# Optimization experiments

Hardware: AMD Instinct MI355X
Metric: run time of the kernel (lower is better)

The kernel has to match this reference:

```python
import jax, jax.numpy as jnp
import numpy as np

B, N, D = 4, 2048, 512
H = 8
DH = D // H
FF = 2 * D


def setup_inputs() -> dict:
    key = jax.random.key(0)
    ks = jax.random.split(key, 16)
    s = lambda fan_in: 1.0 / np.sqrt(fan_in)
    inp = {
        "x0": jax.random.normal(ks[0], (B, N, D), jnp.float32),
        "x1": jax.random.normal(ks[1], (B, N, D), jnp.float32),
        # projections (torch Linear: weight [out, in])
        "Wqk": jax.random.uniform(ks[2], (D, D), jnp.float32, -s(D), s(D)),
        "bqk": jax.random.uniform(ks[3], (D,), jnp.float32, -s(D), s(D)),
        "Wv": jax.random.uniform(ks[4], (D, D), jnp.float32, -s(D), s(D)),
        "bv": jax.random.uniform(ks[5], (D,), jnp.float32, -s(D), s(D)),
        "Wo": jax.random.uniform(ks[6], (D, D), jnp.float32, -s(D), s(D)),
        "bo": jax.random.uniform(ks[7], (D,), jnp.float32, -s(D), s(D)),
        # FFN: Linear(2D,2D) -> LayerNorm(2D) -> GELU -> Linear(2D,D)
        "Wf1": jax.random.uniform(ks[8], (FF, FF), jnp.float32, -s(FF), s(FF)),
        "bf1": jax.random.uniform(ks[9], (FF,), jnp.float32, -s(FF), s(FF)),
        "ln_g": jnp.ones((FF,), jnp.float32),
        "ln_b": jnp.zeros((FF,), jnp.float32),
        "Wf2": jax.random.uniform(ks[10], (D, FF), jnp.float32, -s(FF), s(FF)),
        "bf2": jax.random.uniform(ks[11], (D,), jnp.float32, -s(FF), s(FF)),
    }
    return inp


def _split_heads(t):
    # [B,N,D] -> [B,H,N,DH]
    return t.reshape(B, N, H, DH).transpose(0, 2, 1, 3)


def _attn(q, k, v):
    # q,k,v: [B,H,N,DH]; scale by sqrt(d_k) as in the torch Attention module
    scores = jnp.einsum("bhnd,bhmd->bhnm", q, k) / jnp.sqrt(jnp.float32(DH))
    attn = jax.nn.softmax(scores, axis=-1)
    return jnp.einsum("bhnm,bhmd->bhnd", attn, v)


def _merge_heads(t):
    # [B,H,N,DH] -> [B,N,D]
    return t.transpose(0, 2, 1, 3).reshape(B, N, D)


def _ffn(x, Wf1, bf1, ln_g, ln_b, Wf2, bf2):
    h = x @ Wf1.T + bf1
    mu = jnp.mean(h, axis=-1, keepdims=True)
    var = jnp.mean(jnp.square(h - mu), axis=-1, keepdims=True)
    h = (h - mu) / jnp.sqrt(var + 1e-5) * ln_g + ln_b
    h = jax.nn.gelu(h, approximate=False)
    return h @ Wf2.T + bf2


def reference(x0, x1, Wqk, bqk, Wv, bv, Wo, bo, Wf1, bf1, ln_g, ln_b, Wf2, bf2):
    qk0 = _split_heads(x0 @ Wqk.T + bqk)
    qk1 = _split_heads(x1 @ Wqk.T + bqk)
    v0 = _split_heads(x0 @ Wv.T + bv)
    v1 = _split_heads(x1 @ Wv.T + bv)

    m0 = _merge_heads(_attn(qk0, qk1, v1)) @ Wo.T + bo
    m1 = _merge_heads(_attn(qk1, qk0, v0)) @ Wo.T + bo

    y0 = x0 + _ffn(jnp.concatenate([x0, m0], -1), Wf1, bf1, ln_g, ln_b, Wf2, bf2)
    y1 = x1 + _ffn(jnp.concatenate([x1, m1], -1), Wf1, bf1, ln_g, ln_b, Wf2, bf2)
    return (y0, y1)
```

## Files before the change

### kernel.cpp

```cpp
#include <hip/hip_runtime.h>
#include <hip/hip_bf16.h>
#include <math.h>

typedef __bf16 bf16;
typedef __bf16 bf16x8 __attribute__((ext_vector_type(8)));
typedef __bf16 bf16x4 __attribute__((ext_vector_type(4)));
typedef float  f32x4  __attribute__((ext_vector_type(4)));

#define DEVI __device__ __forceinline__

DEVI void async16(bf16* lds, const bf16* g) {
    __builtin_amdgcn_global_load_lds(
        (const __attribute__((address_space(1))) unsigned int*)g,
        (__attribute__((address_space(3))) unsigned int*)lds, 16, 0, 0);
}
DEVI f32x4 mfma16(bf16x8 a, bf16x8 b, f32x4 c) {
    return __builtin_amdgcn_mfma_f32_16x16x32_bf16(a, b, c, 0, 0, 0);
}

__global__ __launch_bounds__(256) void prep(
    const float* __restrict__ x0, const float* __restrict__ x1, bf16* __restrict__ Xbf,
    const float* __restrict__ Wqk, const float* __restrict__ Wv,
    const float* __restrict__ Wf1, const float* __restrict__ Wf2,
    bf16* __restrict__ Wqkv, bf16* __restrict__ Wbig, bf16* __restrict__ Wf1Rb,
    bf16* __restrict__ Wf2b,
    const float* __restrict__ Wo, bf16* __restrict__ WoT,
    const float* __restrict__ bo, const float* __restrict__ bf1,
    float* __restrict__ bf1p)
{
    __shared__ float Ls[64][65];
    const int bid = blockIdx.x, t = threadIdx.x;
    if (bid < 8192) {
        long i = (long)bid * 256 + t;
        long r = i >> 7, c = (i & 127) * 4;
        const float* src = (r < 8192) ? (x0 + r * 512 + c) : (x1 + (r - 8192) * 512 + c);
        float4 v = *(const float4*)src;
        bf16x4 o;
        o[0] = (bf16)v.x; o[1] = (bf16)v.y; o[2] = (bf16)v.z; o[3] = (bf16)v.w;
        *(bf16x4*)(Xbf + r * 1024 + c) = o;
    } else if (bid < 10240) {
        long i = (long)(bid - 8192) * 256 + t;
        const float* s; bf16* d;
        if (i < 131072) {
            s = (i < 65536) ? Wqk + i * 4 : Wv + (i - 65536) * 4;
            d = Wqkv + i * 4;
        } else if (i < 393216) {
            long e = (i - 131072) * 4, r = e >> 10, c = e & 1023;
            s = Wf1 + e;
            d = (c < 512) ? (Wbig + r * 1024 + c) : (Wf1Rb + r * 512 + (c - 512));
        } else {
            s = Wf2 + (i - 393216) * 4;
            d = Wf2b + (i - 393216) * 4;
        }
        float4 v = *(const float4*)s;
        bf16x4 o;
        o[0] = (bf16)v.x; o[1] = (bf16)v.y; o[2] = (bf16)v.z; o[3] = (bf16)v.w;
        *(bf16x4*)d = o;
    } else if (bid < 10304) {
        const int bb = bid - 10240;
        const int bi = bb & 7, bj = bb >> 3;
        const int i0 = bi * 64, j0 = bj * 64;
        const int r0 = t >> 4, c4 = (t & 15) * 4;
#pragma unroll
        for (int it = 0; it < 4; it++) {
            int row = r0 + 16 * it;
            float4 v = *(const float4*)(Wo + (long)(i0 + row) * 512 + j0 + c4);
            Ls[row][c4] = v.x; Ls[row][c4 + 1] = v.y;
            Ls[row][c4 + 2] = v.z; Ls[row][c4 + 3] = v.w;
        }
        __syncthreads();
#pragma unroll
        for (int it = 0; it < 4; it++) {
            int orow = r0 + 16 * it;
            bf16x4 o;
#pragma unroll
            for (int k = 0; k < 4; k++) o[k] = (bf16)Ls[c4 + k][orow];
            *(bf16x4*)(WoT + (long)(j0 + orow) * 512 + i0 + c4) = o;
        }
    } else {
        const int w = t >> 6, lane = t & 63;
        const int row = (bid - 10304) * 4 + w;
        const float* rp = Wf1 + (long)row * 1024 + 512 + lane * 8;
        float4 a = *(const float4*)rp;
        float4 b = *(const float4*)(rp + 4);
        const float* bp = bo + lane * 8;
        float4 c = *(const float4*)bp;
        float4 d = *(const float4*)(bp + 4);
        float s = a.x * c.x + a.y * c.y + a.z * c.z + a.w * c.w +
                  b.x * d.x + b.y * d.y + b.z * d.z + b.w * d.w;
#pragma unroll
        for (int k = 1; k < 64; k <<= 1) s += __shfl_xor(s, k);
        if (lane == 0) bf1p[row] = bf1[row] + s;
    }
}

template <int MODE>
__global__ __launch_bounds__(256) void gemm_bt(
    const bf16* __restrict__ A, long lda,
    const bf16* __restrict__ B, long ldb,
    const float* __restrict__ bias,
    void* __restrict__ Cout, long ldc,
    const float* __restrict__ res0, const float* __restrict__ res1,
    const float* __restrict__ bias2, void* __restrict__ Cout2,
    int M, int N, int K, float scale)
{
    __shared__ bf16 As[128 * 64];
    __shared__ bf16 Bs[128 * 64];
    const int t = threadIdx.x;
    const int w = t >> 6, lane = t & 63, quad = lane >> 4, m15 = lane & 15;
    const int wm = w >> 1, wn = w & 1;
    const int nbx = N >> 7;
    const int xcd = blockIdx.x & 7, local = blockIdx.x >> 3;
    const int mtiles_per_xcd = (int)(gridDim.x >> 3) / nbx;
    const int by = xcd * mtiles_per_xcd + local / nbx;
    const int bx = local % nbx;
    const long m0 = (long)by * 128, n0 = (long)bx * 128;

    f32x4 acc[4][4] = {};

    for (int k0 = 0; k0 < K; k0 += 64) {
#pragma unroll
        for (int i = 0; i < 4; i++) {
            int idx = i * 256 + t, row = idx >> 3, p = idx & 7;
            int gc = k0 + ((p ^ (row & 7)) * 8);
            async16(As + idx * 8, A + (m0 + row) * lda + gc);
            async16(Bs + idx * 8, B + (n0 + row) * ldb + gc);
        }
        __syncthreads();
#pragma unroll
        for (int kk = 0; kk < 2; kk++) {
            bf16x8 af[4], bfr[4];
#pragma unroll
            for (int mt = 0; mt < 4; mt++) {
                int row = wm * 64 + mt * 16 + m15;
                af[mt] = *(const bf16x8*)(As + row * 64 + (((kk * 4 + quad) ^ (row & 7)) * 8));
            }
#pragma unroll
            for (int nt = 0; nt < 4; nt++) {
                int row = wn * 64 + nt * 16 + m15;
                bfr[nt] = *(const bf16x8*)(Bs + row * 64 + (((kk * 4 + quad) ^ (row & 7)) * 8));
            }
#pragma unroll
            for (int mt = 0; mt < 4; mt++)
#pragma unroll
                for (int nt = 0; nt < 4; nt++)
                    acc[mt][nt] = mfma16(af[mt], bfr[nt], acc[mt][nt]);
        }
        __syncthreads();
    }

#pragma unroll
    for (int nt = 0; nt < 4; nt++) {
        long col = n0 + wn * 64 + nt * 16 + m15;
#pragma unroll
        for (int mt = 0; mt < 4; mt++) {
            long row = m0 + wm * 64 + mt * 16 + quad * 4;
            if (MODE == 0) {
                bf16* C = (bf16*)Cout;
                float bs = bias[col];
#pragma unroll
                for (int r = 0; r < 4; r++)
                    C[(row + r) * ldc + col] = (bf16)(acc[mt][nt][r] + bs);
            } else if (MODE == 4) {
                bf16* C = (bf16*)Cout;
#pragma unroll
                for (int r = 0; r < 4; r++)
                    C[(row + r) * ldc + col] = (bf16)acc[mt][nt][r];
            } else if (MODE == 5) {
                if (col < 512) {
                    bf16* C = (bf16*)Cout;
                    float bs = bias[col];
#pragma unroll
                    for (int r = 0; r < 4; r++)
                        C[(row + r) * ldc + col] = (bf16)((acc[mt][nt][r] + bs) * scale);
                } else {
                    bf16* V = (bf16*)Cout2;
                    long v = col - 512;
                    float bs = bias2[v];
                    bf16x4 pv;
#pragma unroll
                    for (int r = 0; r < 4; r++) pv[r] = (bf16)(acc[mt][nt][r] + bs);
                    *(bf16x4*)(V + v * 16384 + row) = pv;
                }
            } else {
                float* C = (float*)Cout;
                float bs = bias[col];
#pragma unroll
                for (int r = 0; r < 4; r++) {
                    long grow = row + r;
                    const float* rs = (grow < 8192) ? (res0 + grow * 512)
                                                    : (res1 + (grow - 8192) * 512);
                    C[grow * ldc + col] = acc[mt][nt][r] + bs + rs[col];
                }
            }
        }
    }
}

__global__ __launch_bounds__(256, 4) void flash_attn(const bf16* __restrict__ QK,
                                                     const bf16* __restrict__ VT,
                                                     bf16* __restrict__ o)
{
    __shared__ bf16 lds[20480];
    bf16* Ks = lds;
    bf16* Vs = lds + 8192;
    bf16* Ps = lds + 12288;

    const int t = threadIdx.x, w = t >> 6, lane = t & 63;
    const int quad = lane >> 4, m15 = lane & 15;
    const int bid = blockIdx.x;
    const int qt5 = bid & 15;
    const int h   = (bid >> 4) & 7;
    const int b   = (bid >> 7) & 3;
    const int dir = bid >> 9;
    const long qrow0  = (long)dir * 8192 + b * 2048 + qt5 * 128;
    const long kvrow0 = (long)(1 - dir) * 8192 + b * 2048;
    const int hc = h * 64;

#pragma unroll
    for (int i = 0; i < 4; i++) {
        int idx = i * 256 + t, row = idx >> 3, p = idx & 7;
        async16(lds + idx * 8, QK + (qrow0 + row) * 512 + hc + ((p ^ (row & 7)) * 8));
    }
    __syncthreads();
    bf16x8 qf[2][2];
#pragma unroll
    for (int qt = 0; qt < 2; qt++)
#pragma unroll
        for (int kh = 0; kh < 2; kh++) {
            int row = w * 32 + qt * 16 + m15;
            qf[qt][kh] = *(const bf16x8*)(lds + row * 64 + (((kh * 4 + quad) ^ (row & 7)) * 8));
        }
    __syncthreads();

#pragma unroll
    for (int i = 0; i < 2; i++) {
        int idx = i * 256 + t, row = idx >> 3, p = idx & 7;
        async16(Ks + idx * 8, QK + (kvrow0 + row) * 512 + hc + ((p ^ (row & 7)) * 8));
    }

    f32x4 oacc[4][2] = {};
    f32x4 racc[2] = {};
    bf16x8 ones;
#pragma unroll
    for (int j = 0; j < 8; j++) ones[j] = (bf16)1.0f;

    int cur = 0;
    for (int kb = 0; kb < 32; kb++) {
        const long key0  = kvrow0 + kb * 64;
        const long key0n = kvrow0 + ((kb + 1) & 31) * 64;
        bf16* Kc = Ks + cur * 4096;
        bf16* Kn = Ks + (cur ^ 1) * 4096;

        asm volatile("s_waitcnt vmcnt(0)" ::: "memory");
        __builtin_amdgcn_s_barrier();

#pragma unroll
        for (int i = 0; i < 2; i++) {
            int idx = i * 256 + t, row = idx >> 3, p = idx & 7;
            async16(Vs + idx * 8, VT + (long)(hc + row) * 16384 + key0 + ((p ^ (row & 7)) * 8));
        }
#pragma unroll
        for (int i = 0; i < 2; i++) {
            int idx = i * 256 + t, row = idx >> 3, p = idx & 7;
            async16(Kn + idx * 8, QK + (key0n + row) * 512 + hc + ((p ^ (row & 7)) * 8));
        }

        f32x4 s[4][2];
        __builtin_amdgcn_s_setprio(1);
#pragma unroll
        for (int mt = 0; mt < 4; mt++) {
            int row = mt * 16 + m15;
            bf16x8 kf0 = *(const bf16x8*)(Kc + row * 64 + ((quad ^ (row & 7)) * 8));
            bf16x8 kf1 = *(const bf16x8*)(Kc + row * 64 + (((4 + quad) ^ (row & 7)) * 8));
#pragma unroll
            for (int qt = 0; qt < 2; qt++) {
                f32x4 z = {0.f, 0.f, 0.f, 0.f};
                z = mfma16(kf0, qf[qt][0], z);
                s[mt][qt] = mfma16(kf1, qf[qt][1], z);
            }
        }
        __builtin_amdgcn_s_setprio(0);

#pragma unroll
        for (int qt = 0; qt < 2; qt++)
#pragma unroll
            for (int mt = 0; mt < 4; mt++)
#pragma unroll
                for (int r = 0; r < 4; r++)
                    s[mt][qt][r] = exp2f(s[mt][qt][r]);

        bf16* Pw = Ps + w * 2048;
#pragma unroll
        for (int qt = 0; qt < 2; qt++) {
            int ql = qt * 16 + m15;
#pragma unroll
            for (int mt = 0; mt < 4; mt++) {
                bf16x4 pv;
#pragma unroll
                for (int r = 0; r < 4; r++) pv[r] = (bf16)s[mt][qt][r];
                int u = (mt * 2 + (quad >> 1)) ^ (ql & 7);
                *(bf16x4*)(Pw + ql * 64 + u * 8 + (quad & 1) * 4) = pv;
            }
        }
        asm volatile("s_waitcnt vmcnt(2) lgkmcnt(0)" ::: "memory");
        __builtin_amdgcn_s_barrier();

        __builtin_amdgcn_s_setprio(1);
#pragma unroll
        for (int kc = 0; kc < 2; kc++) {
            bf16x8 pf[2];
#pragma unroll
            for (int qt = 0; qt < 2; qt++) {
                int ql = qt * 16 + m15;
                pf[qt] = *(const bf16x8*)(Pw + ql * 64 + (((kc * 4 + quad) ^ (ql & 7)) * 8));
            }
#pragma unroll
            for (int qt = 0; qt < 2; qt++)
                racc[qt] = mfma16(pf[qt], ones, racc[qt]);
#pragma unroll
            for (int dt = 0; dt < 4; dt++) {
                int vrow = dt * 16 + m15;
                bf16x8 vf = *(const bf16x8*)(Vs + vrow * 64 + (((kc * 4 + quad) ^ (vrow & 7)) * 8));
#pragma unroll
                for (int qt = 0; qt < 2; qt++)
                    oacc[dt][qt] = mfma16(pf[qt], vf, oacc[dt][qt]);
            }
        }
        __builtin_amdgcn_s_setprio(0);
        cur ^= 1;
    }

#pragma unroll
    for (int qt = 0; qt < 2; qt++)
#pragma unroll
        for (int r = 0; r < 4; r++) {
            float inv = 1.f / racc[qt][r];
            long row = qrow0 + w * 32 + qt * 16 + quad * 4 + r;
#pragma unroll
            for (int dt = 0; dt < 4; dt++)
                o[row * 1024 + hc + dt * 16 + m15] = (bf16)(oacc[dt][qt][r] * inv);
        }
}

__global__ __launch_bounds__(256) void ln_gelu(bf16* __restrict__ H,
                                               const float* __restrict__ g,
                                               const float* __restrict__ bta)
{
    const int row = blockIdx.x, t = threadIdx.x;
    const int w = t >> 6, lane = t & 63;
    bf16* hp = H + (long)row * 1024 + t * 4;
    bf16x4 hv = *(const bf16x4*)hp;
    float h[4];
#pragma unroll
    for (int j = 0; j < 4; j++) h[j] = (float)hv[j];
    float s1 = h[0] + h[1] + h[2] + h[3];
    float s2 = h[0] * h[0] + h[1] * h[1] + h[2] * h[2] + h[3] * h[3];
#pragma unroll
    for (int d = 1; d < 64; d <<= 1) {
        s1 += __shfl_xor(s1, d);
        s2 += __shfl_xor(s2, d);
    }
    __shared__ float rbuf[8];
    if (lane == 0) { rbuf[w] = s1; rbuf[4 + w] = s2; }
    __syncthreads();
    s1 = rbuf[0] + rbuf[1] + rbuf[2] + rbuf[3];
    s2 = rbuf[4] + rbuf[5] + rbuf[6] + rbuf[7];
    const float mu = s1 * (1.f / 1024.f);
    const float var = s2 * (1.f / 1024.f) - mu * mu;
    const float rstd = rsqrtf(var + 1e-5f);
    bf16x4 out;
#pragma unroll
    for (int j = 0; j < 4; j++) {
        int c = t * 4 + j;
        float x = (h[j] - mu) * rstd * g[c] + bta[c];
        float y = 0.5f * x * (1.f + erff(x * 0.70710678118654752f));
        out[j] = (bf16)y;
    }
    *(bf16x4*)hp = out;
}

extern "C" void kernel_launch(void* const* d_in, const int* in_sizes, int n_in,
                              void* d_out, int out_size, void* d_ws, size_t ws_size,
                              hipStream_t stream)
{
    const float* x0  = (const float*)d_in[0];
    const float* x1  = (const float*)d_in[1];
    const float* Wqk = (const float*)d_in[2];
    const float* bqk = (const float*)d_in[3];
    const float* Wv  = (const float*)d_in[4];
    const float* bv  = (const float*)d_in[5];
    const float* Wo  = (const float*)d_in[6];
    const float* bo  = (const float*)d_in[7];
    const float* Wf1 = (const float*)d_in[8];
    const float* bf1 = (const float*)d_in[9];
    const float* lng = (const float*)d_in[10];
    const float* lnb = (const float*)d_in[11];
    const float* Wf2 = (const float*)d_in[12];
    const float* bf2 = (const float*)d_in[13];

    char* ws = (char*)d_ws;
    bf16* Xbf   = (bf16*)ws; ws += 16384L * 1024 * 2;
    bf16* QKbf  = (bf16*)ws;
    bf16* Hbuf  = (bf16*)ws;
    ws += 16384L * 512 * 2;
    bf16* VtG   = (bf16*)ws; ws += 16384L * 512 * 2;
    bf16* Wqkv  = (bf16*)ws; ws += 1024L * 512 * 2;
    bf16* Wbig  = (bf16*)ws; ws += 1024L * 1024 * 2;
    bf16* Wf1Rb = (bf16*)ws; ws += 1024L * 512 * 2;
    bf16* Wf2b  = (bf16*)ws; ws += 512L * 1024 * 2;
    bf16* WoT   = (bf16*)ws; ws += 512L * 512 * 2;
    float* bf1p = (float*)ws; ws += 1024 * 4;

    const float qs = 0.42466090014400953f;

    prep<<<10560, 256, 0, stream>>>(x0, x1, Xbf, Wqk, Wv, Wf1, Wf2,
                                    Wqkv, Wbig, Wf1Rb, Wf2b, Wo, WoT, bo, bf1, bf1p);

    gemm_bt<4><<<32, 256, 0, stream>>>(Wf1Rb, 512, WoT, 512, nullptr,
                                       Wbig + 512, 1024, nullptr, nullptr,
                                       nullptr, nullptr, 1024, 512, 512, 1.f);

    gemm_bt<5><<<1024, 256, 0, stream>>>(Xbf, 1024, Wqkv, 512, bqk,
                                         QKbf, 512, nullptr, nullptr,
                                         bv, VtG, 16384, 1024, 512, qs);

    flash_attn<<<1024, 256, 0, stream>>>(QKbf, VtG, Xbf + 512);

    gemm_bt<0><<<1024, 256, 0, stream>>>(Xbf, 1024, Wbig, 1024, bf1p,
                                         Hbuf, 1024, nullptr, nullptr,
                                         nullptr, nullptr, 16384, 1024, 1024, 1.f);
    ln_gelu<<<16384, 256, 0, stream>>>(Hbuf, lng, lnb);
    gemm_bt<1><<<512, 256, 0, stream>>>(Hbuf, 1024, Wf2b, 1024, bf2,
                                        d_out, 512, x0, x1,
                                        nullptr, nullptr, 16384, 512, 1024, 1.f);
}
```

Measured before the change: 367.8 us.

## Rewrite flash attention with 32x32 MFMA and register-resident P via permlane swap

The attention kernel moves from 16x16x32 to 32x32x16 bf16 MFMA tiles and doubles the query tile per block to 256 rows, halving the grid. Probabilities are packed with v_cvt_pk_bf16_f32 and rearranged across lane halves with permlane32_swap, so they feed the PV MFMA straight from registers instead of round-tripping through LDS. That removes the mid-iteration barrier. K and V are now double-buffered together with a prologue load, and occupancy drops to 2 blocks per CU. The aim is fewer LDS accesses and syncs and more MFMA work per wave, at the cost of higher register pressure and fewer resident waves.

```diff
diff --git a/kernel.cpp b/kernel.cpp
--- a/kernel.cpp
+++ b/kernel.cpp
@@ -6,6 +6,8 @@
 typedef __bf16 bf16x8 __attribute__((ext_vector_type(8)));
 typedef __bf16 bf16x4 __attribute__((ext_vector_type(4)));
 typedef float  f32x4  __attribute__((ext_vector_type(4)));
+typedef float  f32x16 __attribute__((ext_vector_type(16)));
+typedef unsigned int u32x2 __attribute__((ext_vector_type(2)));
 
 #define DEVI __device__ __forceinline__
 
@@ -16,6 +18,23 @@
 }
 DEVI f32x4 mfma16(bf16x8 a, bf16x8 b, f32x4 c) {
     return __builtin_amdgcn_mfma_f32_16x16x32_bf16(a, b, c, 0, 0, 0);
+}
+DEVI f32x16 mfma32(bf16x8 a, bf16x8 b, f32x16 c) {
+    return __builtin_amdgcn_mfma_f32_32x32x16_bf16(a, b, c, 0, 0, 0);
+}
+DEVI unsigned cvtpk(float lo, float hi) {
+    unsigned r;
+    asm("v_cvt_pk_bf16_f32 %0, %1, %2" : "=v"(r) : "v"(lo), "v"(hi));
+    return r;
+}
+DEVI void pl32(unsigned &a, unsigned &b) {
+    u32x2 r = __builtin_amdgcn_permlane32_swap(a, b, false, false);
+    a = r.x; b = r.y;
+}
+DEVI bf16x8 mk8(unsigned a0, unsigned a1, unsigned b0, unsigned b1) {
+    union { unsigned u[4]; bf16x8 v; } U;
+    U.u[0] = a0; U.u[1] = a1; U.u[2] = b0; U.u[3] = b1;
+    return U.v;
 }
 
 __global__ __launch_bounds__(256) void prep(
@@ -197,149 +216,146 @@
     }
 }
 
-__global__ __launch_bounds__(256, 4) void flash_attn(const bf16* __restrict__ QK,
+__global__ __launch_bounds__(256, 2) void flash_attn(const bf16* __restrict__ QK,
                                                      const bf16* __restrict__ VT,
                                                      bf16* __restrict__ o)
 {
-    __shared__ bf16 lds[20480];
-    bf16* Ks = lds;
-    bf16* Vs = lds + 8192;
-    bf16* Ps = lds + 12288;
+    __shared__ bf16 lds[16384];
 
     const int t = threadIdx.x, w = t >> 6, lane = t & 63;
-    const int quad = lane >> 4, m15 = lane & 15;
-    const int bid = blockIdx.x;
-    const int qt5 = bid & 15;
-    const int h   = (bid >> 4) & 7;
-    const int b   = (bid >> 7) & 3;
-    const int dir = bid >> 9;
-    const long qrow0  = (long)dir * 8192 + b * 2048 + qt5 * 128;
+    const int l31 = lane & 31, hi = lane >> 5;
+    const int j = blockIdx.x;
+    const int hs = j & 63;
+    const int qt = j >> 6;
+    const int h = hs & 7, b = (hs >> 3) & 3, dir = hs >> 5;
+    const long qrow0  = (long)dir * 8192 + b * 2048 + qt * 256;
     const long kvrow0 = (long)(1 - dir) * 8192 + b * 2048;
     const int hc = h * 64;
 
 #pragma unroll
-    for (int i = 0; i < 4; i++) {
+    for (int i = 0; i < 8; i++) {
         int idx = i * 256 + t, row = idx >> 3, p = idx & 7;
         async16(lds + idx * 8, QK + (qrow0 + row) * 512 + hc + ((p ^ (row & 7)) * 8));
     }
     __syncthreads();
-    bf16x8 qf[2][2];
-#pragma unroll
-    for (int qt = 0; qt < 2; qt++)
-#pragma unroll
-        for (int kh = 0; kh < 2; kh++) {
-            int row = w * 32 + qt * 16 + m15;
-            qf[qt][kh] = *(const bf16x8*)(lds + row * 64 + (((kh * 4 + quad) ^ (row & 7)) * 8));
+    bf16x8 qf[2][4];
+#pragma unroll
+    for (int qb = 0; qb < 2; qb++)
+#pragma unroll
+        for (int kd = 0; kd < 4; kd++) {
+            int qrow = w * 64 + qb * 32 + l31;
+            qf[qb][kd] = *(const bf16x8*)(lds + qrow * 64 + (((kd * 2 + hi) ^ (qrow & 7)) * 8));
         }
     __syncthreads();
 
 #pragma unroll
     for (int i = 0; i < 2; i++) {
         int idx = i * 256 + t, row = idx >> 3, p = idx & 7;
-        async16(Ks + idx * 8, QK + (kvrow0 + row) * 512 + hc + ((p ^ (row & 7)) * 8));
-    }
-
-    f32x4 oacc[4][2] = {};
-    f32x4 racc[2] = {};
+        async16(lds + idx * 8, QK + (kvrow0 + row) * 512 + hc + ((p ^ (row & 7)) * 8));
+    }
+#pragma unroll
+    for (int i = 0; i < 2; i++) {
+        int idx = i * 256 + t, row = idx >> 3, p = idx & 7;
+        async16(lds + 8192 + idx * 8, VT + (long)(hc + row) * 16384 + kvrow0 + ((p ^ (row & 7)) * 8));
+    }
+
+    f32x16 oacc[2][2] = {};
+    f32x16 racc[2] = {};
     bf16x8 ones;
 #pragma unroll
-    for (int j = 0; j < 8; j++) ones[j] = (bf16)1.0f;
-
-    int cur = 0;
+    for (int k = 0; k < 8; k++) ones[k] = (bf16)1.0f;
+
     for (int kb = 0; kb < 32; kb++) {
-        const long key0  = kvrow0 + kb * 64;
-        const long key0n = kvrow0 + ((kb + 1) & 31) * 64;
-        bf16* Kc = Ks + cur * 4096;
-        bf16* Kn = Ks + (cur ^ 1) * 4096;
+        bf16* Kc = lds + (kb & 1) * 4096;
+        bf16* Vc = lds + 8192 + (kb & 1) * 4096;
 
         asm volatile("s_waitcnt vmcnt(0)" ::: "memory");
         __builtin_amdgcn_s_barrier();
 
-#pragma unroll
-        for (int i = 0; i < 2; i++) {
-            int idx = i * 256 + t, row = idx >> 3, p = idx & 7;
-            async16(Vs + idx * 8, VT + (long)(hc + row) * 16384 + key0 + ((p ^ (row & 7)) * 8));
-        }
-#pragma unroll
-        for (int i = 0; i < 2; i++) {
-            int idx = i * 256 + t, row = idx >> 3, p = idx & 7;
-            async16(Kn + idx * 8, QK + (key0n + row) * 512 + hc + ((p ^ (row & 7)) * 8));
-        }
-
-        f32x4 s[4][2];
-        __builtin_amdgcn_s_setprio(1);
-#pragma unroll
-        for (int mt = 0; mt < 4; mt++) {
-            int row = mt * 16 + m15;
-            bf16x8 kf0 = *(const bf16x8*)(Kc + row * 64 + ((quad ^ (row & 7)) * 8));
-            bf16x8 kf1 = *(const bf16x8*)(Kc + row * 64 + (((4 + quad) ^ (row & 7)) * 8));
-#pragma unroll
-            for (int qt = 0; qt < 2; qt++) {
-                f32x4 z = {0.f, 0.f, 0.f, 0.f};
-                z = mfma16(kf0, qf[qt][0], z);
-                s[mt][qt] = mfma16(kf1, qf[qt][1], z);
-            }
-        }
-        __builtin_amdgcn_s_setprio(0);
-
-#pragma unroll
-        for (int qt = 0; qt < 2; qt++)
-#pragma unroll
-            for (int mt = 0; mt < 4; mt++)
-#pragma unroll
-                for (int r = 0; r < 4; r++)
-                    s[mt][qt][r] = exp2f(s[mt][qt][r]);
-
-        bf16* Pw = Ps + w * 2048;
-#pragma unroll
-        for (int qt = 0; qt < 2; qt++) {
-            int ql = qt * 16 + m15;
-#pragma unroll
-            for (int mt = 0; mt < 4; mt++) {
-                bf16x4 pv;
-#pragma unroll
-                for (int r = 0; r < 4; r++) pv[r] = (bf16)s[mt][qt][r];
-                int u = (mt * 2 + (quad >> 1)) ^ (ql & 7);
-                *(bf16x4*)(Pw + ql * 64 + u * 8 + (quad & 1) * 4) = pv;
-            }
-        }
-        asm volatile("s_waitcnt vmcnt(2) lgkmcnt(0)" ::: "memory");
-        __builtin_amdgcn_s_barrier();
-
-        __builtin_amdgcn_s_setprio(1);
-#pragma unroll
-        for (int kc = 0; kc < 2; kc++) {
-            bf16x8 pf[2];
-#pragma unroll
-            for (int qt = 0; qt < 2; qt++) {
-                int ql = qt * 16 + m15;
-                pf[qt] = *(const bf16x8*)(Pw + ql * 64 + (((kc * 4 + quad) ^ (ql & 7)) * 8));
-            }
-#pragma unroll
-            for (int qt = 0; qt < 2; qt++)
-                racc[qt] = mfma16(pf[qt], ones, racc[qt]);
-#pragma unroll
-            for (int dt = 0; dt < 4; dt++) {
-                int vrow = dt * 16 + m15;
-                bf16x8 vf = *(const bf16x8*)(Vs + vrow * 64 + (((kc * 4 + quad) ^ (vrow & 7)) * 8));
-#pragma unroll
-                for (int qt = 0; qt < 2; qt++)
-                    oacc[dt][qt] = mfma16(pf[qt], vf, oacc[dt][qt]);
-            }
-        }
-        __builtin_amdgcn_s_setprio(0);
-        cur ^= 1;
-    }
-
-#pragma unroll
-    for (int qt = 0; qt < 2; qt++)
-#pragma unroll
-        for (int r = 0; r < 4; r++) {
-            float inv = 1.f / racc[qt][r];
-            long row = qrow0 + w * 32 + qt * 16 + quad * 4 + r;
-#pragma unroll
-            for (int dt = 0; dt < 4; dt++)
-                o[row * 1024 + hc + dt * 16 + m15] = (bf16)(oacc[dt][qt][r] * inv);
+        if (kb < 31) {
+            const long knext = kvrow0 + (kb + 1) * 64;
+            bf16* Kn = lds + ((kb + 1) & 1) * 4096;
+            bf16* Vn = lds + 8192 + ((kb + 1) & 1) * 4096;
+#pragma unroll
+            for (int i = 0; i < 2; i++) {
+                int idx = i * 256 + t, row = idx >> 3, p = idx & 7;
+                async16(Kn + idx * 8, QK + (knext + row) * 512 + hc + ((p ^ (row & 7)) * 8));
+            }
+#pragma unroll
+            for (int i = 0; i < 2; i++) {
+                int idx = i * 256 + t, row = idx >> 3, p = idx & 7;
+                async16(Vn + idx * 8, VT + (long)(hc + row) * 16384 + knext + ((p ^ (row & 7)) * 8));
+            }
+        }
+
+#pragma unroll
+        for (int kb2 = 0; kb2 < 2; kb2++) {
+            const int krow = kb2 * 32 + l31;
+            const int ksw = krow & 7;
+            bf16x8 kf0 = *(const bf16x8*)(Kc + krow * 64 + (((0 + hi) ^ ksw) * 8));
+            bf16x8 kf1 = *(const bf16x8*)(Kc + krow * 64 + (((2 + hi) ^ ksw) * 8));
+            bf16x8 kf2 = *(const bf16x8*)(Kc + krow * 64 + (((4 + hi) ^ ksw) * 8));
+            bf16x8 kf3 = *(const bf16x8*)(Kc + krow * 64 + (((6 + hi) ^ ksw) * 8));
+
+            f32x16 s0 = {}, s1 = {};
+            __builtin_amdgcn_s_setprio(1);
+            s0 = mfma32(kf0, qf[0][0], s0);
+            s0 = mfma32(kf1, qf[0][1], s0);
+            s0 = mfma32(kf2, qf[0][2], s0);
+            s0 = mfma32(kf3, qf[0][3], s0);
+            s1 = mfma32(kf0, qf[1][0], s1);
+            s1 = mfma32(kf1, qf[1][1], s1);
+            s1 = mfma32(kf2, qf[1][2], s1);
+            s1 = mfma32(kf3, qf[1][3], s1);
+            __builtin_amdgcn_s_setprio(0);
+
+#pragma unroll
+            for (int r = 0; r < 16; r++) {
+                s0[r] = exp2f(s0[r]);
+                s1[r] = exp2f(s1[r]);
+            }
+
+#pragma unroll
+            for (int sh = 0; sh < 2; sh++) {
+                const int ks = kb2 * 2 + sh;
+                unsigned a00 = cvtpk(s0[8 * sh + 0], s0[8 * sh + 1]);
+                unsigned a01 = cvtpk(s0[8 * sh + 2], s0[8 * sh + 3]);
+                unsigned b00 = cvtpk(s0[8 * sh + 4], s0[8 * sh + 5]);
+                unsigned b01 = cvtpk(s0[8 * sh + 6], s0[8 * sh + 7]);
+                pl32(a00, b00); pl32(a01, b01);
+                bf16x8 pa0 = mk8(a00, a01, b00, b01);
+                unsigned a10 = cvtpk(s1[8 * sh + 0], s1[8 * sh + 1]);
+                unsigned a11 = cvtpk(s1[8 * sh + 2], s1[8 * sh + 3]);
+                unsigned b10 = cvtpk(s1[8 * sh + 4], s1[8 * sh + 5]);
+                unsigned b11 = cvtpk(s1[8 * sh + 6], s1[8 * sh + 7]);
+                pl32(a10, b10); pl32(a11, b11);
+                bf16x8 pa1 = mk8(a10, a11, b10, b11);
+
+                __builtin_amdgcn_s_setprio(1);
+#pragma unroll
+                for (int db = 0; db < 2; db++) {
+                    const int vrow = db * 32 + l31;
+                    bf16x8 vf = *(const bf16x8*)(Vc + vrow * 64 + (((ks * 2 + hi) ^ (vrow & 7)) * 8));
+                    oacc[0][db] = mfma32(pa0, vf, oacc[0][db]);
+                    oacc[1][db] = mfma32(pa1, vf, oacc[1][db]);
+                }
+                racc[0] = mfma32(pa0, ones, racc[0]);
+                racc[1] = mfma32(pa1, ones, racc[1]);
+                __builtin_amdgcn_s_setprio(0);
+            }
+        }
+    }
+
+#pragma unroll
+    for (int qb = 0; qb < 2; qb++)
+#pragma unroll
+        for (int reg = 0; reg < 16; reg++) {
+            const int q = (reg & 3) + 8 * (reg >> 2) + 4 * hi;
+            const float inv = 1.f / racc[qb][reg];
+            const long row = qrow0 + w * 64 + qb * 32 + q;
+#pragma unroll
+            for (int db = 0; db < 2; db++)
+                o[row * 1024 + hc + db * 32 + l31] = (bf16)(oacc[qb][db][reg] * inv);
         }
 }
 
@@ -425,7 +441,7 @@
                                          QKbf, 512, nullptr, nullptr,
                                          bv, VtG, 16384, 1024, 512, qs);
 
-    flash_attn<<<1024, 256, 0, stream>>>(QKbf, VtG, Xbf + 512);
+    flash_attn<<<512, 256, 0, stream>>>(QKbf, VtG, Xbf + 512);
 
     gemm_bt<0><<<1024, 256, 0, stream>>>(Xbf, 1024, Wbig, 1024, bf1p,
                                          Hbuf, 1024, nullptr, nullptr,
```

Result: no change. 368.2 us (+0.1%).
